# Optimization experiments

Measured on AMD Instinct MI355X. Metric: run time of the kernel, lower is better.

The kernel has to match this reference:

```python
import jax, jax.numpy as jnp
import numpy as np

X = 32; Y = 32
H1 = (X + Y) * 10 * 8          # 5120
H2 = X * Y * 4                 # 4096
HID = 1 * (X * X + Y * Y)      # gru_scale_s=1 -> 2048
IN1 = 2 * X + Y + X * Y        # 1120
IN2 = 2 * Y + Y + X * Y        # 1120
OUT1 = X * X; OUT2 = Y * Y


def gru_cell(x, h, Wih, Whh, bih, bhh):
    # PyTorch GRU cell, gate order r,z,n
    gi = Wih @ x + bih
    gh = Whh @ h + bhh
    ir, iz, inn = jnp.split(gi, 3)
    hr, hz, hn = jnp.split(gh, 3)
    r = jax.nn.sigmoid(ir + hr)
    z = jax.nn.sigmoid(iz + hz)
    n = jnp.tanh(inn + r * hn)
    return (1.0 - z) * n + z * h


def setup_inputs() -> dict:
    key = jax.random.key(0)
    ks = iter(jax.random.split(key, 40))
    f32 = jnp.float32
    def rn(shape, scale=0.02):
        return (jax.random.normal(next(ks), shape, dtype=f32) * scale)
    inp = {
        'state_inno': rn((X, 1), 1.0),
        'observation_inno': rn((Y, 1), 1.0),
        'diff_state': rn((X, 1), 1.0),
        'diff_obs': rn((Y, 1), 1.0),
        'linearization_error': rn((Y, 1), 1.0),
        'Jacobian': rn((X * Y, 1), 1.0),
        'l1_W': rn((H1, IN1)), 'l1_b': rn((H1,)),
        'gru1_Wih': rn((3 * HID, H1)), 'gru1_Whh': rn((3 * HID, HID)),
        'gru1_bih': rn((3 * HID,)), 'gru1_bhh': rn((3 * HID,)),
        'l2_W1': rn((H2, HID)), 'l2_b1': rn((H2,)),
        'l2_W2': rn((OUT1, H2)), 'l2_b2': rn((OUT1,)),
        'l3_W': rn((H1, IN2)), 'l3_b': rn((H1,)),
        'gru2_Wih': rn((3 * HID, H1)), 'gru2_Whh': rn((3 * HID, HID)),
        'gru2_bih': rn((3 * HID,)), 'gru2_bhh': rn((3 * HID,)),
        'l4_W1': rn((H2, HID)), 'l4_b1': rn((H2,)),
        'l4_W2': rn((OUT2, H2)), 'l4_b2': rn((OUT2,)),
        'hn1': rn((HID,), 1.0),
        'hn2': rn((HID,), 1.0),
    }
    return inp


def reference(state_inno, observation_inno, diff_state, diff_obs,
              linearization_error, Jacobian,
              l1_W, l1_b, gru1_Wih, gru1_Whh, gru1_bih, gru1_bhh,
              l2_W1, l2_b1, l2_W2, l2_b2,
              l3_W, l3_b, gru2_Wih, gru2_Whh, gru2_bih, gru2_bhh,
              l4_W1, l4_b1, l4_W2, l4_b2, hn1, hn2):
    input1 = jnp.concatenate([state_inno, diff_state, linearization_error, Jacobian], axis=0).reshape(-1)
    input2 = jnp.concatenate([observation_inno, diff_obs, linearization_error, Jacobian], axis=0).reshape(-1)

    l1_out = jax.nn.relu(l1_W @ input1 + l1_b)           # [H1]
    h1 = gru_cell(l1_out, hn1, gru1_Wih, gru1_Whh, gru1_bih, gru1_bhh)  # [HID]
    l2_out = l2_W2 @ jax.nn.relu(l2_W1 @ h1 + l2_b1) + l2_b2
    Pk = l2_out.reshape(X, X)

    l3_out = jax.nn.relu(l3_W @ input2 + l3_b)
    h2 = gru_cell(l3_out, hn2, gru2_Wih, gru2_Whh, gru2_bih, gru2_bhh)
    l4_out = l4_W2 @ jax.nn.relu(l4_W1 @ h2 + l4_b1) + l4_b2
    Sk = l4_out.reshape(Y, Y)
    return (Pk, Sk)
```

## Files before the change

### kernel.cpp

```cpp
#include <hip/hip_runtime.h>
#include <hip/hip_bf16.h>

typedef __attribute__((ext_vector_type(4))) float f32x4;

#define TPB 256

#define IN1F   0
#define IN2F   1120
#define HN1F   2240
#define HN2F   4288
#define L1OUT  6336
#define L3OUT  11456
#define GH1    16576
#define GH2    22720
#define GI1    28864
#define GI2    35008
#define H1OFF  41152
#define H2OFF  43200
#define T1OFF  45248
#define T2OFF  49344

__device__ __forceinline__ void matvec_block(
    const float* __restrict__ W,
    const float* __restrict__ bias,
    const float* __restrict__ x, float* xl, int K,
    int row0, int rowsPerWave, float* __restrict__ y, int act)
{
    for (int i = threadIdx.x; i < (K >> 2); i += TPB)
        ((f32x4*)xl)[i] = ((const f32x4*)x)[i];
    __syncthreads();

    const int wid  = threadIdx.x >> 6;
    const int lane = threadIdx.x & 63;
    const int c0   = lane * 4;

    int r = row0 + wid * rowsPerWave;
    for (int i = 0; i < rowsPerWave; ++i, ++r) {
        const float* Wr = W + (size_t)r * K;
        float acc = 0.f;
        for (int kc = 0; kc < K; kc += 256) {
            int c = kc + c0;
            if (c < K) {
                const f32x4 w4 = *reinterpret_cast<const f32x4*>(Wr + c);
                const f32x4 xv = *reinterpret_cast<const f32x4*>(xl + c);
                acc += w4[0] * xv[0] + w4[1] * xv[1]
                     + w4[2] * xv[2] + w4[3] * xv[3];
            }
        }
#pragma unroll
        for (int off = 32; off; off >>= 1) acc += __shfl_xor(acc, off, 64);
        if (lane == 0) {
            float v = acc + bias[r];
            if (act) v = fmaxf(v, 0.f);
            y[r] = v;
        }
    }
}

__global__ void k_prep(const float* __restrict__ state_inno,
                       const float* __restrict__ obs_inno,
                       const float* __restrict__ diff_state,
                       const float* __restrict__ diff_obs,
                       const float* __restrict__ lin_err,
                       const float* __restrict__ jac,
                       const float* __restrict__ hn1,
                       const float* __restrict__ hn2,
                       float* __restrict__ ws)
{
    int i = blockIdx.x * blockDim.x + threadIdx.x;
    if (i < 1120) {
        float v;
        if (i < 32)       v = state_inno[i];
        else if (i < 64)  v = diff_state[i - 32];
        else if (i < 96)  v = lin_err[i - 64];
        else              v = jac[i - 96];
        ws[IN1F + i] = v;
        float v2;
        if (i < 32)       v2 = obs_inno[i];
        else if (i < 64)  v2 = diff_obs[i - 32];
        else              v2 = v;
        ws[IN2F + i] = v2;
    }
    if (i < 2048) {
        ws[HN1F + i] = hn1[i];
        ws[HN2F + i] = hn2[i];
    }
}

__global__ void __launch_bounds__(TPB)
k_stageA(const float* l1_W, const float* l1_b,
         const float* l3_W, const float* l3_b,
         const float* Whh1, const float* bhh1,
         const float* Whh2, const float* bhh2,
         float* ws)
{
    __shared__ float xl[2048];
    int bid = blockIdx.x;
    if (bid < 320)
        matvec_block(l1_W, l1_b, ws + IN1F, xl, 1120, bid * 16, 4, ws + L1OUT, 1);
    else if (bid < 640)
        matvec_block(l3_W, l3_b, ws + IN2F, xl, 1120, (bid - 320) * 16, 4, ws + L3OUT, 1);
    else if (bid < 1024)
        matvec_block(Whh1, bhh1, ws + HN1F, xl, 2048, (bid - 640) * 16, 4, ws + GH1, 0);
    else
        matvec_block(Whh2, bhh2, ws + HN2F, xl, 2048, (bid - 1024) * 16, 4, ws + GH2, 0);
}

__global__ void __launch_bounds__(TPB)
k_stageB(const float* Wih1, const float* bih1,
         const float* Wih2, const float* bih2,
         float* ws)
{
    __shared__ float xl[5120];
    int bid = blockIdx.x;
    if (bid < 384)
        matvec_block(Wih1, bih1, ws + L1OUT, xl, 5120, bid * 16, 4, ws + GI1, 0);
    else
        matvec_block(Wih2, bih2, ws + L3OUT, xl, 5120, (bid - 384) * 16, 4, ws + GI2, 0);
}

__global__ void k_gru(const float* __restrict__ hn1,
                      const float* __restrict__ hn2,
                      float* __restrict__ ws)
{
    int i = blockIdx.x * blockDim.x + threadIdx.x;
    int b = i >> 11, j = i & 2047;
    const float* gi = ws + (b ? GI2 : GI1);
    const float* gh = ws + (b ? GH2 : GH1);
    const float* hn = b ? hn2 : hn1;
    float r = 1.f / (1.f + expf(-(gi[j] + gh[j])));
    float z = 1.f / (1.f + expf(-(gi[2048 + j] + gh[2048 + j])));
    float n = tanhf(gi[4096 + j] + r * gh[4096 + j]);
    float h = (1.f - z) * n + z * hn[j];
    ws[(b ? H2OFF : H1OFF) + j] = h;
}

__global__ void __launch_bounds__(TPB)
k_stageD(const float* W21, const float* b21,
         const float* W41, const float* b41,
         float* ws)
{
    __shared__ float xl[2048];
    int bid = blockIdx.x;
    if (bid < 256)
        matvec_block(W21, b21, ws + H1OFF, xl, 2048, bid * 16, 4, ws + T1OFF, 1);
    else
        matvec_block(W41, b41, ws + H2OFF, xl, 2048, (bid - 256) * 16, 4, ws + T2OFF, 1);
}

__global__ void __launch_bounds__(TPB)
k_stageE(const float* W22, const float* b22,
         const float* W42, const float* b42,
         float* ws, float* out)
{
    __shared__ float xl[4096];
    int bid = blockIdx.x;
    if (bid < 128)
        matvec_block(W22, b22, ws + T1OFF, xl, 4096, bid * 8, 2, out, 0);
    else
        matvec_block(W42, b42, ws + T2OFF, xl, 4096, (bid - 128) * 8, 2, out + 1024, 0);
}

extern "C" void kernel_launch(void* const* d_in, const int* in_sizes, int n_in,
                              void* d_out, int out_size, void* d_ws, size_t ws_size,
                              hipStream_t stream)
{
    const float* state_inno = (const float*)d_in[0];
    const float* obs_inno   = (const float*)d_in[1];
    const float* diff_state = (const float*)d_in[2];
    const float* diff_obs   = (const float*)d_in[3];
    const float* lin_err    = (const float*)d_in[4];
    const float* jac        = (const float*)d_in[5];
    const float* l1_W  = (const float*)d_in[6];
    const float* l1_b  = (const float*)d_in[7];
    const float* g1Wih = (const float*)d_in[8];
    const float* g1Whh = (const float*)d_in[9];
    const float* g1bih = (const float*)d_in[10];
    const float* g1bhh = (const float*)d_in[11];
    const float* l2_W1 = (const float*)d_in[12];
    const float* l2_b1 = (const float*)d_in[13];
    const float* l2_W2 = (const float*)d_in[14];
    const float* l2_b2 = (const float*)d_in[15];
    const float* l3_W  = (const float*)d_in[16];
    const float* l3_b  = (const float*)d_in[17];
    const float* g2Wih = (const float*)d_in[18];
    const float* g2Whh = (const float*)d_in[19];
    const float* g2bih = (const float*)d_in[20];
    const float* g2bhh = (const float*)d_in[21];
    const float* l4_W1 = (const float*)d_in[22];
    const float* l4_b1 = (const float*)d_in[23];
    const float* l4_W2 = (const float*)d_in[24];
    const float* l4_b2 = (const float*)d_in[25];
    const float* hn1   = (const float*)d_in[26];
    const float* hn2   = (const float*)d_in[27];

    float* ws = (float*)d_ws;
    float* out = (float*)d_out;

    hipLaunchKernelGGL(k_prep, dim3(8), dim3(TPB), 0, stream,
                       state_inno, obs_inno, diff_state, diff_obs, lin_err, jac,
                       hn1, hn2, ws);

    hipLaunchKernelGGL(k_stageA, dim3(1408), dim3(TPB), 0, stream,
                       l1_W, l1_b, l3_W, l3_b, g1Whh, g1bhh, g2Whh, g2bhh, ws);

    hipLaunchKernelGGL(k_stageB, dim3(768), dim3(TPB), 0, stream,
                       g1Wih, g1bih, g2Wih, g2bih, ws);

    hipLaunchKernelGGL(k_gru, dim3(16), dim3(TPB), 0, stream, hn1, hn2, ws);

    hipLaunchKernelGGL(k_stageD, dim3(512), dim3(TPB), 0, stream,
                       l2_W1, l2_b1, l4_W1, l4_b1, ws);

    hipLaunchKernelGGL(k_stageE, dim3(256), dim3(TPB), 0, stream,
                       l2_W2, l2_b2, l4_W2, l4_b2, ws, out);
}
```

Before: 106.9 us.

## Split matvec rows across waves with inline-asm burst loads and more blocks

Replaces the generic per-wave row matvec with size-specialised routines. For the wide matrices, each row is split across the four waves and the partial sums are combined through shared memory. Weight loads are issued as back-to-back dwordx4 bursts in inline assembly so several loads are in flight per row. Grids are enlarged so more blocks stream the weights in parallel, aiming to raise memory-level parallelism on this bandwidth-bound workload. In exchange it adds a __syncthreads per row and an explicit vmcnt(0) wait after every burst, which serialises each row's load-then-compute.

```diff
diff --git a/kernel.cpp b/kernel.cpp
--- a/kernel.cpp
+++ b/kernel.cpp
@@ -20,39 +20,184 @@
 #define T1OFF  45248
 #define T2OFF  49344
 
-__device__ __forceinline__ void matvec_block(
-    const float* __restrict__ W,
-    const float* __restrict__ bias,
-    const float* __restrict__ x, float* xl, int K,
-    int row0, int rowsPerWave, float* __restrict__ y, int act)
+
+__device__ __forceinline__ void burst2(const float* a,
+                                       f32x4& w0, f32x4& w1)
+{
+    asm volatile(
+        "global_load_dwordx4 %0, %2, off\n\t"
+        "global_load_dwordx4 %1, %2, off offset:1024\n\t"
+        "s_waitcnt vmcnt(0)"
+        : "=&v"(w0), "=&v"(w1)
+        : "v"(a) : "memory");
+}
+
+__device__ __forceinline__ void burst4(const float* a,
+                                       f32x4& w0, f32x4& w1, f32x4& w2, f32x4& w3)
+{
+    asm volatile(
+        "global_load_dwordx4 %0, %4, off\n\t"
+        "global_load_dwordx4 %1, %4, off offset:1024\n\t"
+        "global_load_dwordx4 %2, %4, off offset:2048\n\t"
+        "global_load_dwordx4 %3, %4, off offset:3072\n\t"
+        "s_waitcnt vmcnt(0)"
+        : "=&v"(w0), "=&v"(w1), "=&v"(w2), "=&v"(w3)
+        : "v"(a) : "memory");
+}
+
+__device__ __forceinline__ void burst5(const float* a, const float* a4,
+                                       f32x4& w0, f32x4& w1, f32x4& w2,
+                                       f32x4& w3, f32x4& w4)
+{
+    asm volatile(
+        "global_load_dwordx4 %0, %5, off\n\t"
+        "global_load_dwordx4 %1, %5, off offset:1024\n\t"
+        "global_load_dwordx4 %2, %5, off offset:2048\n\t"
+        "global_load_dwordx4 %3, %5, off offset:3072\n\t"
+        "global_load_dwordx4 %4, %6, off\n\t"
+        "s_waitcnt vmcnt(0)"
+        : "=&v"(w0), "=&v"(w1), "=&v"(w2), "=&v"(w3), "=&v"(w4)
+        : "v"(a), "v"(a4) : "memory");
+}
+
+__device__ __forceinline__ float dot4(const f32x4& w, const f32x4& x) {
+    return w[0]*x[0] + w[1]*x[1] + w[2]*x[2] + w[3]*x[3];
+}
+
+__device__ __forceinline__ float wave_reduce(float acc) {
+#pragma unroll
+    for (int off = 32; off; off >>= 1) acc += __shfl_xor(acc, off, 64);
+    return acc;
+}
+
+__device__ __forceinline__ void stage_x(const float* __restrict__ x, float* xl, int K)
 {
     for (int i = threadIdx.x; i < (K >> 2); i += TPB)
         ((f32x4*)xl)[i] = ((const f32x4*)x)[i];
     __syncthreads();
-
+}
+
+
+template <int ROWS>
+__device__ __forceinline__ void mv5120(
+    const float* __restrict__ W, const float* __restrict__ bias,
+    float* xl, float* red, int row0, float* __restrict__ y, int act)
+{
     const int wid  = threadIdx.x >> 6;
     const int lane = threadIdx.x & 63;
     const int c0   = lane * 4;
-
-    int r = row0 + wid * rowsPerWave;
-    for (int i = 0; i < rowsPerWave; ++i, ++r) {
-        const float* Wr = W + (size_t)r * K;
-        float acc = 0.f;
-        for (int kc = 0; kc < K; kc += 256) {
-            int c = kc + c0;
-            if (c < K) {
-                const f32x4 w4 = *reinterpret_cast<const f32x4*>(Wr + c);
-                const f32x4 xv = *reinterpret_cast<const f32x4*>(xl + c);
-                acc += w4[0] * xv[0] + w4[1] * xv[1]
-                     + w4[2] * xv[2] + w4[3] * xv[3];
-            }
+    const float* xw = xl + wid * 1280 + c0;
+
+#pragma unroll
+    for (int r = 0; r < ROWS; ++r) {
+        const float* seg = W + (size_t)(row0 + r) * 5120 + wid * 1280 + c0;
+        f32x4 w0, w1, w2, w3, w4;
+        burst5(seg, seg + 1024, w0, w1, w2, w3, w4);
+        float acc = dot4(w0, *reinterpret_cast<const f32x4*>(xw))
+                  + dot4(w1, *reinterpret_cast<const f32x4*>(xw + 256))
+                  + dot4(w2, *reinterpret_cast<const f32x4*>(xw + 512))
+                  + dot4(w3, *reinterpret_cast<const f32x4*>(xw + 768))
+                  + dot4(w4, *reinterpret_cast<const f32x4*>(xw + 1024));
+        acc = wave_reduce(acc);
+        if (lane == 0) red[r * 4 + wid] = acc;
+        __syncthreads();
+    }
+    if (threadIdx.x < ROWS) {
+        int t = threadIdx.x;
+        float v = red[t*4] + red[t*4+1] + red[t*4+2] + red[t*4+3] + bias[row0 + t];
+        if (act) v = fmaxf(v, 0.f);
+        y[row0 + t] = v;
+    }
+}
+
+template <int ROWS>
+__device__ __forceinline__ void mv2048(
+    const float* __restrict__ W, const float* __restrict__ bias,
+    float* xl, float* red, int row0, float* __restrict__ y, int act)
+{
+    const int wid  = threadIdx.x >> 6;
+    const int lane = threadIdx.x & 63;
+    const int c0   = lane * 4;
+    const float* xw = xl + wid * 512 + c0;
+
+#pragma unroll
+    for (int r = 0; r < ROWS; ++r) {
+        const float* seg = W + (size_t)(row0 + r) * 2048 + wid * 512 + c0;
+        f32x4 w0, w1;
+        burst2(seg, w0, w1);
+        float acc = dot4(w0, *reinterpret_cast<const f32x4*>(xw))
+                  + dot4(w1, *reinterpret_cast<const f32x4*>(xw + 256));
+        acc = wave_reduce(acc);
+        if (lane == 0) red[r * 4 + wid] = acc;
+        __syncthreads();
+    }
+    if (threadIdx.x < ROWS) {
+        int t = threadIdx.x;
+        float v = red[t*4] + red[t*4+1] + red[t*4+2] + red[t*4+3] + bias[row0 + t];
+        if (act) v = fmaxf(v, 0.f);
+        y[row0 + t] = v;
+    }
+}
+
+template <int ROWS>
+__device__ __forceinline__ void mv4096(
+    const float* __restrict__ W, const float* __restrict__ bias,
+    float* xl, float* red, int row0, float* __restrict__ y, int act)
+{
+    const int wid  = threadIdx.x >> 6;
+    const int lane = threadIdx.x & 63;
+    const int c0   = lane * 4;
+    const float* xw = xl + wid * 1024 + c0;
+
+#pragma unroll
+    for (int r = 0; r < ROWS; ++r) {
+        const float* seg = W + (size_t)(row0 + r) * 4096 + wid * 1024 + c0;
+        f32x4 w0, w1, w2, w3;
+        burst4(seg, w0, w1, w2, w3);
+        float acc = dot4(w0, *reinterpret_cast<const f32x4*>(xw))
+                  + dot4(w1, *reinterpret_cast<const f32x4*>(xw + 256))
+                  + dot4(w2, *reinterpret_cast<const f32x4*>(xw + 512))
+                  + dot4(w3, *reinterpret_cast<const f32x4*>(xw + 768));
+        acc = wave_reduce(acc);
+        if (lane == 0) red[r * 4 + wid] = acc;
+        __syncthreads();
+    }
+    if (threadIdx.x < ROWS) {
+        int t = threadIdx.x;
+        float v = red[t*4] + red[t*4+1] + red[t*4+2] + red[t*4+3] + bias[row0 + t];
+        if (act) v = fmaxf(v, 0.f);
+        y[row0 + t] = v;
+    }
+}
+
+__device__ __forceinline__ void mv1120(
+    const float* __restrict__ W, const float* __restrict__ bias,
+    float* xl, int row0, float* __restrict__ y, int act)
+{
+    const int wid  = threadIdx.x >> 6;
+    const int lane = threadIdx.x & 63;
+    const int c0   = lane * 4;
+
+#pragma unroll
+    for (int step = 0; step < 2; ++step) {
+        const int rr = row0 + step * 4 + wid;
+        const float* Wr = W + (size_t)rr * 1120;
+        f32x4 w0, w1, w2, w3;
+        burst4(Wr + c0, w0, w1, w2, w3);
+        float acc = dot4(w0, *reinterpret_cast<const f32x4*>(xl + c0))
+                  + dot4(w1, *reinterpret_cast<const f32x4*>(xl + 256 + c0))
+                  + dot4(w2, *reinterpret_cast<const f32x4*>(xl + 512 + c0))
+                  + dot4(w3, *reinterpret_cast<const f32x4*>(xl + 768 + c0));
+        if (c0 < 96) {
+            const f32x4 wt = *reinterpret_cast<const f32x4*>(Wr + 1024 + c0);
+            const f32x4 xt = *reinterpret_cast<const f32x4*>(xl + 1024 + c0);
+            acc += dot4(wt, xt);
         }
-#pragma unroll
-        for (int off = 32; off; off >>= 1) acc += __shfl_xor(acc, off, 64);
+        acc = wave_reduce(acc);
         if (lane == 0) {
-            float v = acc + bias[r];
+            float v = acc + bias[rr];
             if (act) v = fmaxf(v, 0.f);
-            y[r] = v;
+            y[rr] = v;
         }
     }
 }
@@ -95,15 +240,21 @@
          float* ws)
 {
     __shared__ float xl[2048];
+    __shared__ float red[8 * 4];
     int bid = blockIdx.x;
-    if (bid < 320)
-        matvec_block(l1_W, l1_b, ws + IN1F, xl, 1120, bid * 16, 4, ws + L1OUT, 1);
-    else if (bid < 640)
-        matvec_block(l3_W, l3_b, ws + IN2F, xl, 1120, (bid - 320) * 16, 4, ws + L3OUT, 1);
-    else if (bid < 1024)
-        matvec_block(Whh1, bhh1, ws + HN1F, xl, 2048, (bid - 640) * 16, 4, ws + GH1, 0);
-    else
-        matvec_block(Whh2, bhh2, ws + HN2F, xl, 2048, (bid - 1024) * 16, 4, ws + GH2, 0);
+    if (bid < 640) {
+        stage_x(ws + IN1F, xl, 1120);
+        mv1120(l1_W, l1_b, xl, bid * 8, ws + L1OUT, 1);
+    } else if (bid < 1280) {
+        stage_x(ws + IN2F, xl, 1120);
+        mv1120(l3_W, l3_b, xl, (bid - 640) * 8, ws + L3OUT, 1);
+    } else if (bid < 2048) {
+        stage_x(ws + HN1F, xl, 2048);
+        mv2048<8>(Whh1, bhh1, xl, red, (bid - 1280) * 8, ws + GH1, 0);
+    } else {
+        stage_x(ws + HN2F, xl, 2048);
+        mv2048<8>(Whh2, bhh2, xl, red, (bid - 2048) * 8, ws + GH2, 0);
+    }
 }
 
 __global__ void __launch_bounds__(TPB)
@@ -112,11 +263,15 @@
          float* ws)
 {
     __shared__ float xl[5120];
+    __shared__ float red[6 * 4];
     int bid = blockIdx.x;
-    if (bid < 384)
-        matvec_block(Wih1, bih1, ws + L1OUT, xl, 5120, bid * 16, 4, ws + GI1, 0);
-    else
-        matvec_block(Wih2, bih2, ws + L3OUT, xl, 5120, (bid - 384) * 16, 4, ws + GI2, 0);
+    if (bid < 1024) {
+        stage_x(ws + L1OUT, xl, 5120);
+        mv5120<6>(Wih1, bih1, xl, red, bid * 6, ws + GI1, 0);
+    } else {
+        stage_x(ws + L3OUT, xl, 5120);
+        mv5120<6>(Wih2, bih2, xl, red, (bid - 1024) * 6, ws + GI2, 0);
+    }
 }
 
 __global__ void k_gru(const float* __restrict__ hn1,
@@ -141,24 +296,32 @@
          float* ws)
 {
     __shared__ float xl[2048];
+    __shared__ float red[8 * 4];
     int bid = blockIdx.x;
-    if (bid < 256)
-        matvec_block(W21, b21, ws + H1OFF, xl, 2048, bid * 16, 4, ws + T1OFF, 1);
-    else
-        matvec_block(W41, b41, ws + H2OFF, xl, 2048, (bid - 256) * 16, 4, ws + T2OFF, 1);
+    if (bid < 512) {
+        stage_x(ws + H1OFF, xl, 2048);
+        mv2048<8>(W21, b21, xl, red, bid * 8, ws + T1OFF, 1);
+    } else {
+        stage_x(ws + H2OFF, xl, 2048);
+        mv2048<8>(W41, b41, xl, red, (bid - 512) * 8, ws + T2OFF, 1);
+    }
 }
 
 __global__ void __launch_bounds__(TPB)
-k_stageE(const float* W22, const float* b22,
-         const float* W42, const float* b42,
-         float* ws, float* out)
+k_stageE(const float* __restrict__ W22, const float* __restrict__ b22,
+         const float* __restrict__ W42, const float* __restrict__ b42,
+         const float* __restrict__ ws, float* __restrict__ out)
 {
     __shared__ float xl[4096];
+    __shared__ float red[2 * 4];
     int bid = blockIdx.x;
-    if (bid < 128)
-        matvec_block(W22, b22, ws + T1OFF, xl, 4096, bid * 8, 2, out, 0);
-    else
-        matvec_block(W42, b42, ws + T2OFF, xl, 4096, (bid - 128) * 8, 2, out + 1024, 0);
+    if (bid < 512) {
+        stage_x(ws + T1OFF, xl, 4096);
+        mv4096<2>(W22, b22, xl, red, bid * 2, out, 0);
+    } else {
+        stage_x(ws + T2OFF, xl, 4096);
+        mv4096<2>(W42, b42, xl, red, (bid - 512) * 2, out + 1024, 0);
+    }
 }
 
 extern "C" void kernel_launch(void* const* d_in, const int* in_sizes, int n_in,
@@ -201,17 +364,17 @@
                        state_inno, obs_inno, diff_state, diff_obs, lin_err, jac,
                        hn1, hn2, ws);
 
-    hipLaunchKernelGGL(k_stageA, dim3(1408), dim3(TPB), 0, stream,
+    hipLaunchKernelGGL(k_stageA, dim3(2816), dim3(TPB), 0, stream,
                        l1_W, l1_b, l3_W, l3_b, g1Whh, g1bhh, g2Whh, g2bhh, ws);
 
-    hipLaunchKernelGGL(k_stageB, dim3(768), dim3(TPB), 0, stream,
+    hipLaunchKernelGGL(k_stageB, dim3(2048), dim3(TPB), 0, stream,
                        g1Wih, g1bih, g2Wih, g2bih, ws);
 
     hipLaunchKernelGGL(k_gru, dim3(16), dim3(TPB), 0, stream, hn1, hn2, ws);
 
-    hipLaunchKernelGGL(k_stageD, dim3(512), dim3(TPB), 0, stream,
+    hipLaunchKernelGGL(k_stageD, dim3(1024), dim3(TPB), 0, stream,
                        l2_W1, l2_b1, l4_W1, l4_b1, ws);
 
-    hipLaunchKernelGGL(k_stageE, dim3(256), dim3(TPB), 0, stream,
+    hipLaunchKernelGGL(k_stageE, dim3(1024), dim3(TPB), 0, stream,
                        l2_W2, l2_b2, l4_W2, l4_b2, ws, out);
 }
```

Result: no change. 108.6 us (+1.6%).
